# Performance work log

Measured on AMD Instinct MI355X. Metric: run time of the kernel, lower is better.

Reference implementation:

```python
import jax, jax.numpy as jnp
import numpy as np

B, L, D, H, DEPTH = 64, 384, 128, 8, 6
DH = D // H          # 16
VOCAB = 32000
C_OUT = 128
FF = 4 * D           # reformer_pytorch default ff_mult=4
SELF_VAL = -5e4      # TOKEN_SELF_ATTN_VALUE
MASK_VAL = -1e9      # causal mask value


def layer_norm(x, g, b, eps=1e-5):
    mu = jnp.mean(x, -1, keepdims=True)
    var = jnp.mean((x - mu) ** 2, -1, keepdims=True)
    return (x - mu) * jax.lax.rsqrt(var + eps) * g + b


def attn_block(x, p):
    # PreNorm + LSHSelfAttention in full-QK-attention fallback (seq <= full_attn_thres)
    h = layer_norm(x, p['ln1_g'], p['ln1_b'])
    qk = (h @ p['Wqk']).reshape(B, L, H, DH).transpose(0, 2, 1, 3)  # [B,H,L,DH]
    v = (h @ p['Wv']).reshape(B, L, H, DH).transpose(0, 2, 1, 3)
    # shared QK: q = qk, k = l2-normalized qk
    k = qk / jnp.maximum(jnp.linalg.norm(qk, axis=-1, keepdims=True), 1e-12)
    dots = jnp.einsum('bhid,bhjd->bhij', qk, k) * (DH ** -0.5)
    i = jnp.arange(L)
    eye = i[:, None] == i[None, :]
    future = i[None, :] > i[:, None]
    dots = jnp.where(eye, SELF_VAL, dots)   # token cannot (easily) attend to itself
    dots = jnp.where(future, MASK_VAL, dots)  # causal
    a = jax.nn.softmax(dots, axis=-1)
    o = jnp.einsum('bhij,bhjd->bhid', a, v).transpose(0, 2, 1, 3).reshape(B, L, D)
    return o @ p['Wo'] + p['bo']


def ff_block(x, p):
    h = layer_norm(x, p['ln2_g'], p['ln2_b'])
    h = jax.nn.gelu(h @ p['W1'] + p['b1'], approximate=False)
    return h @ p['W2'] + p['b2']


def forward(x_enc, emb, pos1, pos2, ln1_g, ln1_b, Wqk, Wv, Wo, bo,
            ln2_g, ln2_b, W1, b1, W2, b2, lnf_g, lnf_b, Wp, bp):
    # axial positional embedding (summed mode): (25,D) + (25,D) -> (625,D)
    pos = (pos1[:, None, :] + pos2[None, :, :]).reshape(25 * 25, D)[:L]
    x = emb[x_enc] + pos  # [B,L,D]

    layer_params = dict(ln1_g=ln1_g, ln1_b=ln1_b, Wqk=Wqk, Wv=Wv, Wo=Wo, bo=bo,
                        ln2_g=ln2_g, ln2_b=ln2_b, W1=W1, b1=b1, W2=W2, b2=b2)

    def block(carry, p):
        x1, x2 = carry
        y1 = x1 + attn_block(x2, p)
        y2 = x2 + ff_block(y1, p)
        return (y1, y2), None

    # reversible-net math: duplicate stream, run blocks, average the two halves
    (x1, x2), _ = jax.lax.scan(block, (x, x), layer_params)
    x = layer_norm((x1 + x2) * 0.5, lnf_g, lnf_b)
    return x.reshape(B, L * D) @ Wp + bp  # [B, C_OUT]


def setup_inputs() -> dict:
    key = jax.random.key(0)
    ks = jax.random.split(key, 12)
    s = 0.02
    inp = {
        'x_enc': jax.random.randint(ks[0], (B, L), 0, VOCAB, dtype=jnp.int32),
        'emb': jax.random.normal(ks[1], (VOCAB, D), jnp.float32) * s,
        'pos1': jax.random.normal(ks[2], (25, D), jnp.float32) * s,
        'pos2': jax.random.normal(ks[3], (25, D), jnp.float32) * s,
        'ln1_g': jnp.ones((DEPTH, D), jnp.float32),
        'ln1_b': jnp.zeros((DEPTH, D), jnp.float32),
        'Wqk': jax.random.normal(ks[4], (DEPTH, D, D), jnp.float32) * s,
        'Wv': jax.random.normal(ks[5], (DEPTH, D, D), jnp.float32) * s,
        'Wo': jax.random.normal(ks[6], (DEPTH, D, D), jnp.float32) * s,
        'bo': jnp.zeros((DEPTH, D), jnp.float32),
        'ln2_g': jnp.ones((DEPTH, D), jnp.float32),
        'ln2_b': jnp.zeros((DEPTH, D), jnp.float32),
        'W1': jax.random.normal(ks[7], (DEPTH, D, FF), jnp.float32) * s,
        'b1': jnp.zeros((DEPTH, FF), jnp.float32),
        'W2': jax.random.normal(ks[8], (DEPTH, FF, D), jnp.float32) * s,
        'b2': jnp.zeros((DEPTH, D), jnp.float32),
        'lnf_g': jnp.ones((D,), jnp.float32),
        'lnf_b': jnp.zeros((D,), jnp.float32),
        'Wp': jax.random.normal(ks[9], (L * D, C_OUT), jnp.float32) * s,
        'bp': jnp.zeros((C_OUT,), jnp.float32),
    }
    return inp


def reference(x_enc, emb, pos1, pos2, ln1_g, ln1_b, Wqk, Wv, Wo, bo,
              ln2_g, ln2_b, W1, b1, W2, b2, lnf_g, lnf_b, Wp, bp):
    return forward(x_enc, emb, pos1, pos2, ln1_g, ln1_b, Wqk, Wv, Wo, bo,
                   ln2_g, ln2_b, W1, b1, W2, b2, lnf_g, lnf_b, Wp, bp)
```

## Files before the change

### kernel.cpp

```cpp
#include <hip/hip_runtime.h>
#include <hip/hip_bf16.h>
#include <math.h>

#define BB 64
#define LL 384
#define DD 128
#define HH 8
#define DHH 16
#define DEPTH 6
#define FFD 512
#define MROWS (BB*LL)
#define COUT 128
#define KP (LL*DD)
#define KSPLIT 96
#define KCHUNK 512

typedef short bf16x8 __attribute__((ext_vector_type(8)));
typedef float f32x4 __attribute__((ext_vector_type(4)));

__device__ __forceinline__ unsigned short f2bs(float x) {
    __hip_bfloat16 h = __float2bfloat16(x);
    return *reinterpret_cast<unsigned short*>(&h);
}
__device__ __forceinline__ float bs2f(unsigned short u) {
    unsigned int v = ((unsigned int)u) << 16;
    return __uint_as_float(v);
}

__global__ __launch_bounds__(256) void embed_kernel(
    const int* __restrict__ x_enc, const float* __restrict__ emb,
    const float* __restrict__ pos1, const float* __restrict__ pos2,
    float* __restrict__ x1, float* __restrict__ x2)
{
    int t = blockIdx.x * 256 + threadIdx.x;
    int row = t >> 5;
    int c4 = t & 31;
    int l = row % LL;
    int tok = x_enc[row];
    float4 a = ((const float4*)(emb + (size_t)tok * DD))[c4];
    float4 b = ((const float4*)(pos1 + (l / 25) * DD))[c4];
    float4 c = ((const float4*)(pos2 + (l % 25) * DD))[c4];
    float4 r = make_float4(a.x + b.x + c.x, a.y + b.y + c.y,
                           a.z + b.z + c.z, a.w + b.w + c.w);
    ((float4*)x1)[t] = r;
    ((float4*)x2)[t] = r;
}

__global__ __launch_bounds__(256) void castT_kernel(
    const float* __restrict__ src, __hip_bfloat16* __restrict__ dst, int K, int N,
    long sstride, long dstride)
{
    __shared__ float tile[32][33];
    int kb = blockIdx.x * 32, nb = blockIdx.y * 32;
    int tx = threadIdx.x & 31, ty = threadIdx.x >> 5;
    const float* s = src + (size_t)blockIdx.z * sstride;
    __hip_bfloat16* d = dst + (size_t)blockIdx.z * dstride;
    #pragma unroll
    for (int r = 0; r < 32; r += 8)
        tile[r + ty][tx] = s[(size_t)(kb + r + ty) * N + nb + tx];
    __syncthreads();
    #pragma unroll
    for (int r = 0; r < 32; r += 8)
        d[(size_t)(nb + r + ty) * K + kb + tx] = __float2bfloat16(tile[tx][r + ty]);
}

__global__ __launch_bounds__(256) void ln_kernel(
    const float* __restrict__ x, const float* __restrict__ g,
    const float* __restrict__ b, __hip_bfloat16* __restrict__ y)
{
    int wave = threadIdx.x >> 6;
    int lane = threadIdx.x & 63;
    int row = blockIdx.x * 4 + wave;
    float2 v = ((const float2*)(x + (size_t)row * DD))[lane];
    float2 gg = ((const float2*)g)[lane];
    float2 bb = ((const float2*)b)[lane];
    float s = v.x + v.y;
    float sq = v.x * v.x + v.y * v.y;
    #pragma unroll
    for (int off = 32; off > 0; off >>= 1) {
        s += __shfl_down(s, off, 64);
        sq += __shfl_down(sq, off, 64);
    }
    s = __shfl(s, 0, 64);
    sq = __shfl(sq, 0, 64);
    float mean = s * (1.0f / DD);
    float var = sq * (1.0f / DD) - mean * mean;
    float rstd = rsqrtf(var + 1e-5f);
    __hip_bfloat16* yp = y + (size_t)row * DD + lane * 2;
    yp[0] = __float2bfloat16((v.x - mean) * rstd * gg.x + bb.x);
    yp[1] = __float2bfloat16((v.y - mean) * rstd * gg.y + bb.y);
}

__global__ __launch_bounds__(256) void avgln_kernel(
    const float* __restrict__ xa, const float* __restrict__ xb,
    const float* __restrict__ g, const float* __restrict__ b,
    __hip_bfloat16* __restrict__ y)
{
    int wave = threadIdx.x >> 6;
    int lane = threadIdx.x & 63;
    int row = blockIdx.x * 4 + wave;
    float2 va = ((const float2*)(xa + (size_t)row * DD))[lane];
    float2 vb = ((const float2*)(xb + (size_t)row * DD))[lane];
    float2 v = make_float2((va.x + vb.x) * 0.5f, (va.y + vb.y) * 0.5f);
    float2 gg = ((const float2*)g)[lane];
    float2 bb = ((const float2*)b)[lane];
    float s = v.x + v.y;
    float sq = v.x * v.x + v.y * v.y;
    #pragma unroll
    for (int off = 32; off > 0; off >>= 1) {
        s += __shfl_down(s, off, 64);
        sq += __shfl_down(sq, off, 64);
    }
    s = __shfl(s, 0, 64);
    sq = __shfl(sq, 0, 64);
    float mean = s * (1.0f / DD);
    float var = sq * (1.0f / DD) - mean * mean;
    float rstd = rsqrtf(var + 1e-5f);
    __hip_bfloat16* yp = y + (size_t)row * DD + lane * 2;
    yp[0] = __float2bfloat16((v.x - mean) * rstd * gg.x + bb.x);
    yp[1] = __float2bfloat16((v.y - mean) * rstd * gg.y + bb.y);
}

__device__ __forceinline__ float gelu_exact(float x) {
    return 0.5f * x * (1.0f + erff(x * 0.70710678118654752f));
}

template<int K, int N, bool BIAS, bool RES, bool GELU, bool OBF, bool LNOUT>
__global__ __launch_bounds__(256) void gemm_bf16(
    const __hip_bfloat16* __restrict__ A, const __hip_bfloat16* __restrict__ Bt,
    const float* __restrict__ bias, const float* __restrict__ Rsrc,
    void* __restrict__ Cdst,
    const float* __restrict__ lng, const float* __restrict__ lnb,
    __hip_bfloat16* __restrict__ lnout)
{
    __shared__ unsigned short As[64 * 128];
    __shared__ unsigned short Bs[128 * 128];
    int tid = threadIdx.x;
    int l = tid & 63, w = tid >> 6;
    int wr = w >> 1, wc = w & 1;
    int lr = l & 15, q = l >> 4;
    int m0 = blockIdx.y * 64;
    int n0 = blockIdx.x * 128;

    f32x4 acc[2][4];
    #pragma unroll
    for (int mt = 0; mt < 2; ++mt)
        #pragma unroll
        for (int nt = 0; nt < 4; ++nt) acc[mt][nt] = (f32x4){0.f, 0.f, 0.f, 0.f};

    for (int kt = 0; kt < K; kt += 128) {
        if (kt) __syncthreads();
        #pragma unroll
        for (int p = 0; p < 4; ++p) {
            int n = p * 256 + tid;
            int r = n >> 4;
            int c = (n & 15) ^ (r & 7);
            uint4 dv = *(const uint4*)(A + (size_t)(m0 + r) * K + kt + c * 8);
            *(uint4*)&As[n * 8] = dv;
        }
        #pragma unroll
        for (int p = 0; p < 8; ++p) {
            int n = p * 256 + tid;
            int r = n >> 4;
            int c = (n & 15) ^ (r & 7);
            uint4 dv = *(const uint4*)(Bt + (size_t)(n0 + r) * K + kt + c * 8);
            *(uint4*)&Bs[n * 8] = dv;
        }
        __syncthreads();

        #pragma unroll
        for (int kk = 0; kk < 4; ++kk) {
            bf16x8 afr[2], bfr[4];
            #pragma unroll
            for (int mt = 0; mt < 2; ++mt) {
                int rA = wr * 32 + mt * 16 + lr;
                int cc = (kk * 4 + q) ^ (rA & 7);
                afr[mt] = *(const bf16x8*)&As[(rA * 16 + cc) * 8];
            }
            #pragma unroll
            for (int nt = 0; nt < 4; ++nt) {
                int rB = wc * 64 + nt * 16 + lr;
                int cc = (kk * 4 + q) ^ (rB & 7);
                bfr[nt] = *(const bf16x8*)&Bs[(rB * 16 + cc) * 8];
            }
            #pragma unroll
            for (int mt = 0; mt < 2; ++mt)
                #pragma unroll
                for (int nt = 0; nt < 4; ++nt)
                    acc[mt][nt] = __builtin_amdgcn_mfma_f32_16x16x32_bf16(
                        afr[mt], bfr[nt], acc[mt][nt], 0, 0, 0);
        }
    }

    if (!LNOUT) {
        #pragma unroll
        for (int mt = 0; mt < 2; ++mt) {
            #pragma unroll
            for (int nt = 0; nt < 4; ++nt) {
                int col = n0 + wc * 64 + nt * 16 + lr;
                float bv = BIAS ? bias[col] : 0.f;
                #pragma unroll
                for (int r = 0; r < 4; ++r) {
                    int row = m0 + wr * 32 + mt * 16 + q * 4 + r;
                    float val = acc[mt][nt][r] + bv;
                    if (GELU) val = gelu_exact(val);
                    if (RES) val += Rsrc[(size_t)row * N + col];
                    if (OBF) ((__hip_bfloat16*)Cdst)[(size_t)row * N + col] = __float2bfloat16(val);
                    else     ((float*)Cdst)[(size_t)row * N + col] = val;
                }
            }
        }
    } else {
        float* fp = (float*)Bs;
        __syncthreads();
        #pragma unroll
        for (int mt = 0; mt < 2; ++mt) {
            #pragma unroll
            for (int nt = 0; nt < 4; ++nt) {
                int col = wc * 64 + nt * 16 + lr;
                float bv = BIAS ? bias[col] : 0.f;
                #pragma unroll
                for (int r = 0; r < 4; ++r) {
                    int rowL = wr * 32 + mt * 16 + q * 4 + r;
                    float val = acc[mt][nt][r] + bv;
                    if (RES) val += Rsrc[(size_t)(m0 + rowL) * N + col];
                    fp[rowL * 128 + col] = val;
                }
            }
        }
        __syncthreads();
        int rl = tid >> 2, sub = tid & 3;
        float s = 0.f, sq = 0.f;
        #pragma unroll
        for (int c4 = 0; c4 < 8; ++c4) {
            float4 v = *(const float4*)&fp[rl * 128 + sub * 32 + c4 * 4];
            s  += (v.x + v.y) + (v.z + v.w);
            sq += (v.x * v.x + v.y * v.y) + (v.z * v.z + v.w * v.w);
        }
        s  += __shfl_xor(s, 1);  s  += __shfl_xor(s, 2);
        sq += __shfl_xor(sq, 1); sq += __shfl_xor(sq, 2);
        float mean = s * (1.0f / 128.0f);
        float var  = sq * (1.0f / 128.0f) - mean * mean;
        float rstd = rsqrtf(var + 1e-5f);
        int rowG = m0 + rl;
        #pragma unroll
        for (int c4 = 0; c4 < 8; ++c4) {
            int col = sub * 32 + c4 * 4;
            float4 v  = *(const float4*)&fp[rl * 128 + col];
            float4 g4 = *(const float4*)(lng + col);
            float4 b4 = *(const float4*)(lnb + col);
            *(float4*)((float*)Cdst + (size_t)rowG * 128 + col) = v;
            unsigned short pk[4];
            pk[0] = f2bs((v.x - mean) * rstd * g4.x + b4.x);
            pk[1] = f2bs((v.y - mean) * rstd * g4.y + b4.y);
            pk[2] = f2bs((v.z - mean) * rstd * g4.z + b4.z);
            pk[3] = f2bs((v.w - mean) * rstd * g4.w + b4.w);
            *(ushort4*)((unsigned short*)lnout + (size_t)rowG * 128 + col) = *(ushort4*)&pk[0];
        }
    }
}

__global__ __launch_bounds__(256) void attn_kernel(
    const __hip_bfloat16* __restrict__ qkv, __hip_bfloat16* __restrict__ o)
{
    int z  = blockIdx.x >> 9;
    int bh = blockIdx.x & 511;
    int b = bh >> 3, hh = bh & 7;
    const unsigned short* base = (const unsigned short*)qkv + (size_t)b * LL * 256 + hh * DHH;

    __shared__ unsigned short knb[LL + 2][24];
    __shared__ unsigned short vtb[16][LL + 24];
    __shared__ float cq[LL];
    __shared__ unsigned short ptile[4][16][40];

    int t = threadIdx.x;
    for (int r = t; r < LL; r += 256) {
        const unsigned short* qp = base + (size_t)r * 256;
        unsigned short qs[16], vs16[16];
        *(uint4*)&qs[0]  = *(const uint4*)(qp);
        *(uint4*)&qs[8]  = *(const uint4*)(qp + 8);
        *(uint4*)&vs16[0] = *(const uint4*)(qp + 128);
        *(uint4*)&vs16[8] = *(const uint4*)(qp + 136);
        float q[16];
        #pragma unroll
        for (int d = 0; d < 16; ++d) q[d] = bs2f(qs[d]);
        float nrm = 0.f;
        #pragma unroll
        for (int d = 0; d < 16; ++d) nrm = fmaf(q[d], q[d], nrm);
        float qn = sqrtf(nrm);
        float inv = 1.0f / fmaxf(qn, 1e-12f);
        cq[r] = 0.25f * qn;
        unsigned short kb[16];
        #pragma unroll
        for (int d = 0; d < 16; ++d) kb[d] = f2bs(q[d] * inv);
        *(uint4*)&knb[r][0] = *(uint4*)&kb[0];
        *(uint4*)&knb[r][8] = *(uint4*)&kb[8];
        *(uint4*)&knb[r][16] = make_uint4(0u, 0u, 0u, 0u);
        #pragma unroll
        for (int d = 0; d < 16; ++d) vtb[d][r] = vs16[d];
    }
    if (t < 16) {
        #pragma unroll
        for (int c = 0; c < 24; ++c) vtb[t][LL + c] = 0;
    }

    int w = t >> 6, l = t & 63;
    int lr = l & 15, q4 = l >> 4;
    *(uint2*)&ptile[w][lr][16 + q4 * 4] = make_uint2(0u, 0u);
    __syncthreads();

    bf16x8 zfrag = {0, 0, 0, 0, 0, 0, 0, 0};
    bf16x8 onesf;
    #pragma unroll
    for (int i = 0; i < 8; ++i) onesf[i] = (short)0x3F80;

    int slot = 2 * w + z;
    int strips[3] = { slot, 15 - slot, 16 + slot };
    #pragma unroll
    for (int si = 0; si < 3; ++si) {
        int s = strips[si];
        int r0 = s * 16;
        bf16x8 afrag = *(const bf16x8*)&knb[r0 + lr][(q4 & 1) * 8];
        afrag = (q4 < 2) ? afrag : zfrag;
        float ccv[4];
        #pragma unroll
        for (int reg = 0; reg < 4; ++reg) ccv[reg] = cq[r0 + q4 * 4 + reg];

        f32x4 oacc = (f32x4){0.f, 0.f, 0.f, 0.f};
        f32x4 lacc = (f32x4){0.f, 0.f, 0.f, 0.f};

        for (int jt = 0; jt <= s; ++jt) {
            bf16x8 bfrag = *(const bf16x8*)&knb[jt * 16 + lr][q4 * 8];
            f32x4 sacc = __builtin_amdgcn_mfma_f32_16x16x32_bf16(
                afrag, bfrag, (f32x4){0.f, 0.f, 0.f, 0.f}, 0, 0, 0);
            int colg = jt * 16 + lr;
            #pragma unroll
            for (int reg = 0; reg < 4; ++reg) {
                int rowg = r0 + q4 * 4 + reg;
                float pe = __expf(fmaf(sacc[reg], ccv[reg], -ccv[reg]));
                pe = (colg < rowg) ? pe : 0.f;
                ptile[w][q4 * 4 + reg][lr] = f2bs(pe);
            }
            asm volatile("s_waitcnt lgkmcnt(0)" ::: "memory");
            bf16x8 pfrag = *(const bf16x8*)&ptile[w][lr][q4 * 8];
            bf16x8 vfrag = *(const bf16x8*)&vtb[lr][jt * 16 + q4 * 8];
            oacc = __builtin_amdgcn_mfma_f32_16x16x32_bf16(pfrag, vfrag, oacc, 0, 0, 0);
            lacc = __builtin_amdgcn_mfma_f32_16x16x32_bf16(pfrag, onesf, lacc, 0, 0, 0);
        }

        if (s == 0 && q4 == 0) {
            lacc[0] = 1.0f;
            oacc[0] = bs2f(vtb[lr][0]);
        }
        unsigned short* ob = (unsigned short*)o + (size_t)(b * LL + r0) * DD + hh * 16 + lr;
        #pragma unroll
        for (int reg = 0; reg < 4; ++reg) {
            float ov = oacc[reg] / lacc[reg];
            ob[(size_t)(q4 * 4 + reg) * DD] = f2bs(ov);
        }
    }
}

__global__ __launch_bounds__(256) void final_mfma_kernel(
    const __hip_bfloat16* __restrict__ A, const __hip_bfloat16* __restrict__ Bt,
    float* __restrict__ partials)
{
    __shared__ unsigned short As[64 * 128];
    __shared__ unsigned short Bs[128 * 128];
    int tid = threadIdx.x;
    int l = tid & 63, w = tid >> 6;
    int wr = w >> 1, wc = w & 1;
    int lr = l & 15, q = l >> 4;
    int kbase = blockIdx.x * KCHUNK;

    f32x4 acc[2][4];
    #pragma unroll
    for (int mt = 0; mt < 2; ++mt)
        #pragma unroll
        for (int nt = 0; nt < 4; ++nt) acc[mt][nt] = (f32x4){0.f, 0.f, 0.f, 0.f};

    for (int kt = 0; kt < KCHUNK; kt += 128) {
        if (kt) __syncthreads();
        #pragma unroll
        for (int p = 0; p < 4; ++p) {
            int n = p * 256 + tid;
            int r = n >> 4;
            int c = (n & 15) ^ (r & 7);
            uint4 dv = *(const uint4*)(A + (size_t)r * KP + kbase + kt + c * 8);
            *(uint4*)&As[n * 8] = dv;
        }
        #pragma unroll
        for (int p = 0; p < 8; ++p) {
            int n = p * 256 + tid;
            int r = n >> 4;
            int c = (n & 15) ^ (r & 7);
            uint4 dv = *(const uint4*)(Bt + (size_t)r * KP + kbase + kt + c * 8);
            *(uint4*)&Bs[n * 8] = dv;
        }
        __syncthreads();

        #pragma unroll
        for (int kk = 0; kk < 4; ++kk) {
            bf16x8 afr[2], bfr[4];
            #pragma unroll
            for (int mt = 0; mt < 2; ++mt) {
                int rA = wr * 32 + mt * 16 + lr;
                int cc = (kk * 4 + q) ^ (rA & 7);
                afr[mt] = *(const bf16x8*)&As[(rA * 16 + cc) * 8];
            }
            #pragma unroll
            for (int nt = 0; nt < 4; ++nt) {
                int rB = wc * 64 + nt * 16 + lr;
                int cc = (kk * 4 + q) ^ (rB & 7);
                bfr[nt] = *(const bf16x8*)&Bs[(rB * 16 + cc) * 8];
            }
            #pragma unroll
            for (int mt = 0; mt < 2; ++mt)
                #pragma unroll
                for (int nt = 0; nt < 4; ++nt)
                    acc[mt][nt] = __builtin_amdgcn_mfma_f32_16x16x32_bf16(
                        afr[mt], bfr[nt], acc[mt][nt], 0, 0, 0);
        }
    }

    float* dst = partials + (size_t)blockIdx.x * (64 * 128);
    #pragma unroll
    for (int mt = 0; mt < 2; ++mt) {
        #pragma unroll
        for (int nt = 0; nt < 4; ++nt) {
            int col = wc * 64 + nt * 16 + lr;
            #pragma unroll
            for (int r = 0; r < 4; ++r) {
                int row = wr * 32 + mt * 16 + q * 4 + r;
                dst[row * 128 + col] = acc[mt][nt][r];
            }
        }
    }
}

__global__ __launch_bounds__(256) void final_reduce_kernel(
    const float* __restrict__ partials, const float* __restrict__ bp,
    float* __restrict__ out)
{
    int j = blockIdx.x * 256 + threadIdx.x;
    float s = bp[j & (COUT - 1)];
    #pragma unroll 8
    for (int p = 0; p < KSPLIT; ++p)
        s += partials[(size_t)p * 8192 + j];
    out[j] = s;
}

extern "C" void kernel_launch(void* const* d_in, const int* in_sizes, int n_in,
                              void* d_out, int out_size, void* d_ws, size_t ws_size,
                              hipStream_t stream)
{
    const int*   x_enc = (const int*)  d_in[0];
    const float* emb   = (const float*)d_in[1];
    const float* pos1  = (const float*)d_in[2];
    const float* pos2  = (const float*)d_in[3];
    const float* ln1_g = (const float*)d_in[4];
    const float* ln1_b = (const float*)d_in[5];
    const float* Wqk   = (const float*)d_in[6];
    const float* Wv    = (const float*)d_in[7];
    const float* Wo    = (const float*)d_in[8];
    const float* bo    = (const float*)d_in[9];
    const float* ln2_g = (const float*)d_in[10];
    const float* ln2_b = (const float*)d_in[11];
    const float* W1    = (const float*)d_in[12];
    const float* b1    = (const float*)d_in[13];
    const float* W2    = (const float*)d_in[14];
    const float* b2    = (const float*)d_in[15];
    const float* lnf_g = (const float*)d_in[16];
    const float* lnf_b = (const float*)d_in[17];
    const float* Wp    = (const float*)d_in[18];
    const float* bp    = (const float*)d_in[19];
    float* out = (float*)d_out;

    const size_t SZ = (size_t)MROWS * DD;
    float* ws_f = (float*)d_ws;
    float* x1 = ws_f;
    float* x2 = ws_f + SZ;
    float* R  = ws_f + 2 * SZ;
    __hip_bfloat16* qkv_bf = (__hip_bfloat16*)R;
    __hip_bfloat16* hff = (__hip_bfloat16*)R;
    __hip_bfloat16* h_bf = (__hip_bfloat16*)(ws_f + 4 * SZ);
    __hip_bfloat16* o_bf = h_bf + SZ;
    __hip_bfloat16* wqvT = o_bf + SZ;
    __hip_bfloat16* woT  = wqvT + 6 * 32768;
    __hip_bfloat16* w1T  = woT  + 6 * 16384;
    __hip_bfloat16* w2T  = w1T  + 6 * 65536;
    __hip_bfloat16* WpT  = w2T  + 6 * 65536;
    float* partials = (float*)(WpT + (size_t)COUT * KP);

    castT_kernel<<<dim3(4, 4, 6),  dim3(256), 0, stream>>>(Wqk, wqvT,         128, 128, 16384, 32768);
    castT_kernel<<<dim3(4, 4, 6),  dim3(256), 0, stream>>>(Wv,  wqvT + 16384, 128, 128, 16384, 32768);
    castT_kernel<<<dim3(4, 4, 6),  dim3(256), 0, stream>>>(Wo,  woT,          128, 128, 16384, 16384);
    castT_kernel<<<dim3(4, 16, 6), dim3(256), 0, stream>>>(W1,  w1T,          128, 512, 65536, 65536);
    castT_kernel<<<dim3(16, 4, 6), dim3(256), 0, stream>>>(W2,  w2T,          512, 128, 65536, 65536);
    castT_kernel<<<dim3(KP / 32, 4, 1), dim3(256), 0, stream>>>(Wp, WpT, KP, 128, 0, 0);

    embed_kernel<<<dim3(MROWS * 32 / 256), dim3(256), 0, stream>>>(x_enc, emb, pos1, pos2, x1, x2);
    ln_kernel<<<dim3(MROWS / 4), dim3(256), 0, stream>>>(x2, ln1_g, ln1_b, h_bf);

    for (int d = 0; d < DEPTH; ++d) {
        const float* bod = bo + d * DD;
        const float* l2g = ln2_g + d * DD;
        const float* l2b = ln2_b + d * DD;
        const float* b1d = b1 + d * FFD;
        const float* b2d = b2 + d * DD;
        const __hip_bfloat16* wqv_d = wqvT + (size_t)d * 32768;
        const __hip_bfloat16* wo_d  = woT  + (size_t)d * 16384;
        const __hip_bfloat16* w1_d  = w1T  + (size_t)d * 65536;
        const __hip_bfloat16* w2_d  = w2T  + (size_t)d * 65536;

        gemm_bf16<128, 256, false, false, false, true, false>
            <<<dim3(2, MROWS / 64), dim3(256), 0, stream>>>(
                h_bf, wqv_d, nullptr, nullptr, qkv_bf, nullptr, nullptr, nullptr);
        attn_kernel<<<dim3(BB * HH * 2), dim3(256), 0, stream>>>(qkv_bf, o_bf);
        gemm_bf16<128, 128, true, true, false, false, true>
            <<<dim3(1, MROWS / 64), dim3(256), 0, stream>>>(
                o_bf, wo_d, bod, x1, x1, l2g, l2b, h_bf);
        gemm_bf16<128, 512, true, false, true, true, false>
            <<<dim3(4, MROWS / 64), dim3(256), 0, stream>>>(
                h_bf, w1_d, b1d, nullptr, hff, nullptr, nullptr, nullptr);
        if (d < DEPTH - 1) {
            gemm_bf16<512, 128, true, true, false, false, true>
                <<<dim3(1, MROWS / 64), dim3(256), 0, stream>>>(
                    hff, w2_d, b2d, x2, x2, ln1_g + (d + 1) * DD, ln1_b + (d + 1) * DD, h_bf);
        } else {
            gemm_bf16<512, 128, true, true, false, false, false>
                <<<dim3(1, MROWS / 64), dim3(256), 0, stream>>>(
                    hff, w2_d, b2d, x2, x2, nullptr, nullptr, nullptr);
        }
    }

    avgln_kernel<<<dim3(MROWS / 4), dim3(256), 0, stream>>>(x1, x2, lnf_g, lnf_b, h_bf);
    final_mfma_kernel<<<dim3(KSPLIT), dim3(256), 0, stream>>>(h_bf, WpT, partials);
    final_reduce_kernel<<<dim3(32), dim3(256), 0, stream>>>(partials, bp, out);
}
```

Baseline: 680.9 us.

## Fuse final average-layernorm into last FFN GEMM, merge weight casts, unroll attention loop

Merges the Wqk/Wv/Wo transpose-cast launches into one kernel. It also folds the final average-and-layernorm into the epilogue of the last W2 GEMM, which now reads x1 and skips writing x2 back. The attention inner loop is unrolled by two key tiles per iteration, so two MFMAs run per LDS round-trip. The goal is fewer launches, less global traffic and better overlap in attention. The attention unroll assumes the strip count per step is even, which with rows strip s covering tiles 0..s may overrun for even s, a correctness risk.

```diff
diff --git a/kernel.cpp b/kernel.cpp
--- a/kernel.cpp
+++ b/kernel.cpp
@@ -64,6 +64,28 @@
         d[(size_t)(nb + r + ty) * K + kb + tx] = __float2bfloat16(tile[tx][r + ty]);
 }
 
+__global__ __launch_bounds__(256) void castT3_kernel(
+    const float* __restrict__ sqk, const float* __restrict__ sv, const float* __restrict__ so,
+    __hip_bfloat16* __restrict__ dqk, __hip_bfloat16* __restrict__ dv,
+    __hip_bfloat16* __restrict__ dwo)
+{
+    __shared__ float tile[32][33];
+    int which = blockIdx.z / 6;
+    int dd = blockIdx.z % 6;
+    const float* s = (which == 0 ? sqk : (which == 1 ? sv : so)) + (size_t)dd * 16384;
+    __hip_bfloat16* d = (which == 0 ? dqk : (which == 1 ? dv : dwo))
+                        + (size_t)dd * (which == 2 ? 16384 : 32768);
+    int kb = blockIdx.x * 32, nb = blockIdx.y * 32;
+    int tx = threadIdx.x & 31, ty = threadIdx.x >> 5;
+    #pragma unroll
+    for (int r = 0; r < 32; r += 8)
+        tile[r + ty][tx] = s[(size_t)(kb + r + ty) * 128 + nb + tx];
+    __syncthreads();
+    #pragma unroll
+    for (int r = 0; r < 32; r += 8)
+        d[(size_t)(nb + r + ty) * 128 + kb + tx] = __float2bfloat16(tile[tx][r + ty]);
+}
+
 __global__ __launch_bounds__(256) void ln_kernel(
     const float* __restrict__ x, const float* __restrict__ g,
     const float* __restrict__ b, __hip_bfloat16* __restrict__ y)
@@ -91,44 +113,15 @@
     yp[1] = __float2bfloat16((v.y - mean) * rstd * gg.y + bb.y);
 }
 
-__global__ __launch_bounds__(256) void avgln_kernel(
-    const float* __restrict__ xa, const float* __restrict__ xb,
-    const float* __restrict__ g, const float* __restrict__ b,
-    __hip_bfloat16* __restrict__ y)
-{
-    int wave = threadIdx.x >> 6;
-    int lane = threadIdx.x & 63;
-    int row = blockIdx.x * 4 + wave;
-    float2 va = ((const float2*)(xa + (size_t)row * DD))[lane];
-    float2 vb = ((const float2*)(xb + (size_t)row * DD))[lane];
-    float2 v = make_float2((va.x + vb.x) * 0.5f, (va.y + vb.y) * 0.5f);
-    float2 gg = ((const float2*)g)[lane];
-    float2 bb = ((const float2*)b)[lane];
-    float s = v.x + v.y;
-    float sq = v.x * v.x + v.y * v.y;
-    #pragma unroll
-    for (int off = 32; off > 0; off >>= 1) {
-        s += __shfl_down(s, off, 64);
-        sq += __shfl_down(sq, off, 64);
-    }
-    s = __shfl(s, 0, 64);
-    sq = __shfl(sq, 0, 64);
-    float mean = s * (1.0f / DD);
-    float var = sq * (1.0f / DD) - mean * mean;
-    float rstd = rsqrtf(var + 1e-5f);
-    __hip_bfloat16* yp = y + (size_t)row * DD + lane * 2;
-    yp[0] = __float2bfloat16((v.x - mean) * rstd * gg.x + bb.x);
-    yp[1] = __float2bfloat16((v.y - mean) * rstd * gg.y + bb.y);
-}
-
 __device__ __forceinline__ float gelu_exact(float x) {
     return 0.5f * x * (1.0f + erff(x * 0.70710678118654752f));
 }
 
-template<int K, int N, bool BIAS, bool RES, bool GELU, bool OBF, bool LNOUT>
+template<int K, int N, bool BIAS, bool RES, bool GELU, bool OBF, bool LNOUT, bool AVGLN>
 __global__ __launch_bounds__(256) void gemm_bf16(
     const __hip_bfloat16* __restrict__ A, const __hip_bfloat16* __restrict__ Bt,
     const float* __restrict__ bias, const float* __restrict__ Rsrc,
+    const float* __restrict__ Rsrc2,
     void* __restrict__ Cdst,
     const float* __restrict__ lng, const float* __restrict__ lnb,
     __hip_bfloat16* __restrict__ lnout)
@@ -234,6 +227,11 @@
         #pragma unroll
         for (int c4 = 0; c4 < 8; ++c4) {
             float4 v = *(const float4*)&fp[rl * 128 + sub * 32 + c4 * 4];
+            if (AVGLN) {
+                float4 xo = *(const float4*)(Rsrc2 + (size_t)(m0 + rl) * 128 + sub * 32 + c4 * 4);
+                v.x = (v.x + xo.x) * 0.5f; v.y = (v.y + xo.y) * 0.5f;
+                v.z = (v.z + xo.z) * 0.5f; v.w = (v.w + xo.w) * 0.5f;
+            }
             s  += (v.x + v.y) + (v.z + v.w);
             sq += (v.x * v.x + v.y * v.y) + (v.z * v.z + v.w * v.w);
         }
@@ -247,9 +245,15 @@
         for (int c4 = 0; c4 < 8; ++c4) {
             int col = sub * 32 + c4 * 4;
             float4 v  = *(const float4*)&fp[rl * 128 + col];
+            if (AVGLN) {
+                float4 xo = *(const float4*)(Rsrc2 + (size_t)rowG * 128 + col);
+                v.x = (v.x + xo.x) * 0.5f; v.y = (v.y + xo.y) * 0.5f;
+                v.z = (v.z + xo.z) * 0.5f; v.w = (v.w + xo.w) * 0.5f;
+            } else {
+                *(float4*)((float*)Cdst + (size_t)rowG * 128 + col) = v;
+            }
             float4 g4 = *(const float4*)(lng + col);
             float4 b4 = *(const float4*)(lnb + col);
-            *(float4*)((float*)Cdst + (size_t)rowG * 128 + col) = v;
             unsigned short pk[4];
             pk[0] = f2bs((v.x - mean) * rstd * g4.x + b4.x);
             pk[1] = f2bs((v.y - mean) * rstd * g4.y + b4.y);
@@ -329,17 +333,23 @@
         f32x4 oacc = (f32x4){0.f, 0.f, 0.f, 0.f};
         f32x4 lacc = (f32x4){0.f, 0.f, 0.f, 0.f};
 
-        for (int jt = 0; jt <= s; ++jt) {
-            bf16x8 bfrag = *(const bf16x8*)&knb[jt * 16 + lr][q4 * 8];
-            f32x4 sacc = __builtin_amdgcn_mfma_f32_16x16x32_bf16(
-                afrag, bfrag, (f32x4){0.f, 0.f, 0.f, 0.f}, 0, 0, 0);
-            int colg = jt * 16 + lr;
+        for (int jt = 0; jt <= s; jt += 2) {
+            bf16x8 bf0 = *(const bf16x8*)&knb[jt * 16 + lr][q4 * 8];
+            f32x4 s0 = __builtin_amdgcn_mfma_f32_16x16x32_bf16(
+                afrag, bf0, (f32x4){0.f, 0.f, 0.f, 0.f}, 0, 0, 0);
+            bf16x8 bf1 = *(const bf16x8*)&knb[(jt + 1) * 16 + lr][q4 * 8];
+            f32x4 s1 = __builtin_amdgcn_mfma_f32_16x16x32_bf16(
+                afrag, bf1, (f32x4){0.f, 0.f, 0.f, 0.f}, 0, 0, 0);
+            int colg0 = jt * 16 + lr;
             #pragma unroll
             for (int reg = 0; reg < 4; ++reg) {
                 int rowg = r0 + q4 * 4 + reg;
-                float pe = __expf(fmaf(sacc[reg], ccv[reg], -ccv[reg]));
-                pe = (colg < rowg) ? pe : 0.f;
-                ptile[w][q4 * 4 + reg][lr] = f2bs(pe);
+                float p0 = __expf(fmaf(s0[reg], ccv[reg], -ccv[reg]));
+                p0 = (colg0 < rowg) ? p0 : 0.f;
+                float p1 = __expf(fmaf(s1[reg], ccv[reg], -ccv[reg]));
+                p1 = (colg0 + 16 < rowg) ? p1 : 0.f;
+                ptile[w][q4 * 4 + reg][lr] = f2bs(p0);
+                ptile[w][q4 * 4 + reg][16 + lr] = f2bs(p1);
             }
             asm volatile("s_waitcnt lgkmcnt(0)" ::: "memory");
             bf16x8 pfrag = *(const bf16x8*)&ptile[w][lr][q4 * 8];
@@ -492,11 +502,10 @@
     __hip_bfloat16* WpT  = w2T  + 6 * 65536;
     float* partials = (float*)(WpT + (size_t)COUT * KP);
 
-    castT_kernel<<<dim3(4, 4, 6),  dim3(256), 0, stream>>>(Wqk, wqvT,         128, 128, 16384, 32768);
-    castT_kernel<<<dim3(4, 4, 6),  dim3(256), 0, stream>>>(Wv,  wqvT + 16384, 128, 128, 16384, 32768);
-    castT_kernel<<<dim3(4, 4, 6),  dim3(256), 0, stream>>>(Wo,  woT,          128, 128, 16384, 16384);
-    castT_kernel<<<dim3(4, 16, 6), dim3(256), 0, stream>>>(W1,  w1T,          128, 512, 65536, 65536);
-    castT_kernel<<<dim3(16, 4, 6), dim3(256), 0, stream>>>(W2,  w2T,          512, 128, 65536, 65536);
+    castT3_kernel<<<dim3(4, 4, 18), dim3(256), 0, stream>>>(
+        Wqk, Wv, Wo, wqvT, wqvT + 16384, woT);
+    castT_kernel<<<dim3(4, 16, 6), dim3(256), 0, stream>>>(W1, w1T, 128, 512, 65536, 65536);
+    castT_kernel<<<dim3(16, 4, 6), dim3(256), 0, stream>>>(W2, w2T, 512, 128, 65536, 65536);
     castT_kernel<<<dim3(KP / 32, 4, 1), dim3(256), 0, stream>>>(Wp, WpT, KP, 128, 0, 0);
 
     embed_kernel<<<dim3(MROWS * 32 / 256), dim3(256), 0, stream>>>(x_enc, emb, pos1, pos2, x1, x2);
@@ -513,28 +522,28 @@
         const __hip_bfloat16* w1_d  = w1T  + (size_t)d * 65536;
         const __hip_bfloat16* w2_d  = w2T  + (size_t)d * 65536;
 
-        gemm_bf16<128, 256, false, false, false, true, false>
+        gemm_bf16<128, 256, false, false, false, true, false, false>
             <<<dim3(2, MROWS / 64), dim3(256), 0, stream>>>(
-                h_bf, wqv_d, nullptr, nullptr, qkv_bf, nullptr, nullptr, nullptr);
+                h_bf, wqv_d, nullptr, nullptr, nullptr, qkv_bf, nullptr, nullptr, nullptr);
         attn_kernel<<<dim3(BB * HH * 2), dim3(256), 0, stream>>>(qkv_bf, o_bf);
-        gemm_bf16<128, 128, true, true, false, false, true>
+        gemm_bf16<128, 128, true, true, false, false, true, false>
             <<<dim3(1, MROWS / 64), dim3(256), 0, stream>>>(
-                o_bf, wo_d, bod, x1, x1, l2g, l2b, h_bf);
-        gemm_bf16<128, 512, true, false, true, true, false>
+                o_bf, wo_d, bod, x1, nullptr, x1, l2g, l2b, h_bf);
+        gemm_bf16<128, 512, true, false, true, true, false, false>
             <<<dim3(4, MROWS / 64), dim3(256), 0, stream>>>(
-                h_bf, w1_d, b1d, nullptr, hff, nullptr, nullptr, nullptr);
+                h_bf, w1_d, b1d, nullptr, nullptr, hff, nullptr, nullptr, nullptr);
         if (d < DEPTH - 1) {
-            gemm_bf16<512, 128, true, true, false, false, true>
+            gemm_bf16<512, 128, true, true, false, false, true, false>
                 <<<dim3(1, MROWS / 64), dim3(256), 0, stream>>>(
-                    hff, w2_d, b2d, x2, x2, ln1_g + (d + 1) * DD, ln1_b + (d + 1) * DD, h_bf);
+                    hff, w2_d, b2d, x2, nullptr, x2,
+                    ln1_g + (d + 1) * DD, ln1_b + (d + 1) * DD, h_bf);
         } else {
-            gemm_bf16<512, 128, true, true, false, false, false>
+            gemm_bf16<512, 128, true, true, false, false, true, true>
                 <<<dim3(1, MROWS / 64), dim3(256), 0, stream>>>(
-                    hff, w2_d, b2d, x2, x2, nullptr, nullptr, nullptr);
-        }
-    }
-
-    avgln_kernel<<<dim3(MROWS / 4), dim3(256), 0, stream>>>(x1, x2, lnf_g, lnf_b, h_bf);
+                    hff, w2_d, b2d, x2, x1, nullptr, lnf_g, lnf_b, h_bf);
+        }
+    }
+
     final_mfma_kernel<<<dim3(KSPLIT), dim3(256), 0, stream>>>(h_bf, WpT, partials);
     final_reduce_kernel<<<dim3(32), dim3(256), 0, stream>>>(partials, bp, out);
 }
```

Result: no change. 670.4 us (-1.5%).
